# Kernel optimization log

Hardware: AMD Instinct MI355X
Metric: run time of the kernel (lower is better)

The kernel has to match this reference:

```python
import jax, jax.numpy as jnp
import numpy as np

B, C, D = 1024, 100000, 512
S_SCALE, MARGIN, EPS = 64.0, 0.5, 1e-7  # arcface defaults


def setup_inputs() -> dict:
    key = jax.random.key(0)
    kx, kl, kw = jax.random.split(key, 3)
    x = jax.random.normal(kx, (B, D), dtype=jnp.float32)
    labels = jax.random.randint(kl, (B,), 0, C, dtype=jnp.int64)
    # nn.Linear default init: U(-1/sqrt(fan_in), 1/sqrt(fan_in))
    bound = 1.0 / np.sqrt(D)
    W = jax.random.uniform(kw, (C, D), dtype=jnp.float32, minval=-bound, maxval=bound)
    return {"x": x, "labels": labels, "W": W}


def reference(x, labels, W):
    # L2-normalize features (W is NOT normalized in the original -- the
    # normalize loop there rebinds a local and is a no-op).
    xn = x / jnp.maximum(jnp.linalg.norm(x, axis=1, keepdims=True), 1e-12)
    wf = jnp.einsum('bd,cd->bc', xn, W)               # [B, C] cosine-like logits
    target = jnp.take_along_axis(wf, labels[:, None], axis=1)[:, 0]  # [B]
    # arcface: s * cos(acos(clamp(cos_theta)) + m)
    numerator = S_SCALE * jnp.cos(
        jnp.arccos(jnp.clip(target, -1.0 + EPS, 1.0 - EPS)) + MARGIN)
    # sum over excluded classes = full sum - label term
    excl_sum = jnp.sum(jnp.exp(S_SCALE * wf), axis=1) - jnp.exp(S_SCALE * target)
    L = numerator - jnp.log(jnp.exp(numerator) + excl_sum)
    return -jnp.mean(L)
```

## Files before the change

### kernel.cpp

```cpp
#include <hip/hip_runtime.h>
#include <hip/hip_bf16.h>
#include <math.h>

#define NB 1024
#define NC 100000
#define ND 512
#define SSCALE 64.0f
#define MMARGIN 0.5f

#define BM 256
#define BN 128
#define BK 32
#define NKS (ND / BK)
#define NRT (NB / BM)
#define NCT ((NC + BN - 1) / BN)
#define GRIDSZ (NRT * NCT)

#define ABASE 0
#define ABUF  16384
#define BBASE 32768
#define BBUF  8192

typedef __bf16 bf16x8 __attribute__((ext_vector_type(8)));
typedef float f32x4 __attribute__((ext_vector_type(4)));

__device__ __forceinline__ void gload_lds16(const void* g, void* l) {
    __builtin_amdgcn_global_load_lds(
        (const __attribute__((address_space(1))) unsigned int*)g,
        (__attribute__((address_space(3))) unsigned int*)l, 16, 0, 0);
}


__global__ void prep_kernel(const float* __restrict__ x, __bf16* __restrict__ xnb) {
    const int row = blockIdx.x;
    const int tid = threadIdx.x;
    const float2 v = *reinterpret_cast<const float2*>(x + (size_t)row * ND + tid * 2);
    float ss = v.x * v.x + v.y * v.y;
#pragma unroll
    for (int m = 1; m < 64; m <<= 1) ss += __shfl_xor(ss, m);
    __shared__ float wsum[4];
    if ((tid & 63) == 0) wsum[tid >> 6] = ss;
    __syncthreads();
    const float tot = wsum[0] + wsum[1] + wsum[2] + wsum[3];
    const float inv = 1.0f / fmaxf(sqrtf(tot), 1e-12f);
    __bf16* dst = xnb + (size_t)row * ND + tid * 2;
    dst[0] = (__bf16)(v.x * inv);
    dst[1] = (__bf16)(v.y * inv);
}

__global__ void target_kernel(const __bf16* __restrict__ xnb, const float* __restrict__ Wg,
                              const int* __restrict__ labels, float* __restrict__ tgt) {
    const int wid  = threadIdx.x >> 6;
    const int lane = threadIdx.x & 63;
    const int row  = blockIdx.x * 4 + wid;
    const int lab  = labels[row];
    const int k    = lane * 8;
    const bf16x8 xv = *reinterpret_cast<const bf16x8*>(xnb + (size_t)row * ND + k);
    const float* wr = Wg + (size_t)lab * ND + k;
    const float4 w0 = *reinterpret_cast<const float4*>(wr);
    const float4 w1 = *reinterpret_cast<const float4*>(wr + 4);
    float s = (float)xv[0] * w0.x + (float)xv[1] * w0.y + (float)xv[2] * w0.z + (float)xv[3] * w0.w
            + (float)xv[4] * w1.x + (float)xv[5] * w1.y + (float)xv[6] * w1.z + (float)xv[7] * w1.w;
#pragma unroll
    for (int m = 1; m < 64; m <<= 1) s += __shfl_xor(s, m);
    if (lane == 0) tgt[row] = s;
}

__global__ __launch_bounds__(512, 4) void gemm_exp_kernel(const __bf16* __restrict__ xnb,
                                                          const float* __restrict__ Wg,
                                                          float* __restrict__ sums) {
    __shared__ char lds[49152];
    const int tid  = threadIdx.x;
    const int wid  = tid >> 6;
    const int lane = tid & 63;
    const int l15  = lane & 15;
    const int lhi  = lane >> 4;
    const int wr   = wid >> 1;
    const int wc   = wid & 1;

    const int logical = (blockIdx.x & 7) * (GRIDSZ / 8) + (blockIdx.x >> 3);
    const int rt = logical & 3;
    const int ct = logical >> 2;
    const int r0 = rt * BM;
    const int c0 = ct * BN;

    const int bcls = tid >> 2;
    const int bqk  = tid & 3;
    const bool bok = (c0 + bcls) < NC;
    float4 bw0, bw1;
    auto loadB = [&](int t) {
        if (bok) {
            const float* src = Wg + (size_t)(c0 + bcls) * ND + t * BK + bqk * 8;
            bw0 = *reinterpret_cast<const float4*>(src);
            bw1 = *reinterpret_cast<const float4*>(src + 4);
        } else {
            bw0 = make_float4(0.f, 0.f, 0.f, 0.f);
            bw1 = bw0;
        }
    };
    auto writeB = [&](int buf) {
        struct alignas(16) bf8s { __bf16 h[8]; };
        bf8s h;
        h.h[0] = (__bf16)bw0.x; h.h[1] = (__bf16)bw0.y; h.h[2] = (__bf16)bw0.z; h.h[3] = (__bf16)bw0.w;
        h.h[4] = (__bf16)bw1.x; h.h[5] = (__bf16)bw1.y; h.h[6] = (__bf16)bw1.z; h.h[7] = (__bf16)bw1.w;
        const int ck = bqk ^ ((bcls >> 1) & 3);
        *reinterpret_cast<bf8s*>(lds + BBASE + buf * BBUF + bcls * 64 + (ck << 4)) = h;
    };

    auto stageA = [&](int t, int buf) {
#pragma unroll
        for (int s = 0; s < 2; ++s) {
            const int lin = s * 8192 + wid * 1024 + (lane << 4);
            const int row = lin >> 6;
            const int cnk = (lin >> 4) & 3;
            const int sc  = cnk ^ ((row >> 1) & 3);
            const char* src = (const char*)xnb + (size_t)(r0 + row) * 1024 + t * 64 + sc * 16;
            gload_lds16(src, lds + ABASE + buf * ABUF + s * 8192 + wid * 1024);
        }
    };

    f32x4 acc[4][4] = {};

    auto compute = [&](int buf) {
        bf16x8 a[4], b[4];
#pragma unroll
        for (int i = 0; i < 4; ++i) {
            const int r = wr * 64 + i * 16 + l15;
            const int ck = lhi ^ ((r >> 1) & 3);
            a[i] = *reinterpret_cast<const bf16x8*>(lds + ABASE + buf * ABUF + r * 64 + (ck << 4));
        }
#pragma unroll
        for (int j = 0; j < 4; ++j) {
            const int cls = wc * 64 + j * 16 + l15;
            const int ck  = lhi ^ ((cls >> 1) & 3);
            b[j] = *reinterpret_cast<const bf16x8*>(lds + BBASE + buf * BBUF + cls * 64 + (ck << 4));
        }
#pragma unroll
        for (int i = 0; i < 4; ++i)
#pragma unroll
            for (int j = 0; j < 4; ++j)
                acc[i][j] = __builtin_amdgcn_mfma_f32_16x16x32_bf16(a[i], b[j], acc[i][j], 0, 0, 0);
    };

    loadB(0);
    stageA(0, 0);
    writeB(0);
    __syncthreads();

#pragma unroll 1
    for (int t = 0; t < NKS; ++t) {
        const int buf = t & 1;
        if (t + 1 < NKS) {
            loadB(t + 1);
            stageA(t + 1, buf ^ 1);
        }
        compute(buf);
        if (t + 1 < NKS) writeB(buf ^ 1);
        __syncthreads();
    }

#pragma unroll
    for (int i = 0; i < 4; ++i) {
#pragma unroll
        for (int r = 0; r < 4; ++r) {
            float v = 0.f;
#pragma unroll
            for (int j = 0; j < 4; ++j) {
                const int c = c0 + wc * 64 + j * 16 + l15;
                v += (c < NC) ? __expf(SSCALE * acc[i][j][r]) : 0.f;
            }
            v += __shfl_xor(v, 1);
            v += __shfl_xor(v, 2);
            v += __shfl_xor(v, 4);
            v += __shfl_xor(v, 8);
            if (l15 == 0) {
                const int row = r0 + wr * 64 + i * 16 + lhi * 4 + r;
                atomicAdd(&sums[row], v);
            }
        }
    }
}

__global__ void finalize_kernel(const float* __restrict__ sums, const float* __restrict__ tgt,
                                float* __restrict__ out) {
    const int tid  = threadIdx.x;
    const int wid  = tid >> 6;
    const int lane = tid & 63;
    float t  = tgt[tid];
    const float se = sums[tid];
    t = fminf(fmaxf(t, -1.0f + 1e-7f), 1.0f - 1e-7f);
    const float numer = SSCALE * cosf(acosf(t) + MMARGIN);
    const float excl  = se - expf(SSCALE * t);
    float L = numer - logf(expf(numer) + excl);
#pragma unroll
    for (int m = 1; m < 64; m <<= 1) L += __shfl_xor(L, m);
    __shared__ float ws2[16];
    if (lane == 0) ws2[wid] = L;
    __syncthreads();
    if (tid == 0) {
        float tot = 0.f;
        for (int i = 0; i < 16; ++i) tot += ws2[i];
        out[0] = -(tot / (float)NB);
    }
}

extern "C" void kernel_launch(void* const* d_in, const int* in_sizes, int n_in,
                              void* d_out, int out_size, void* d_ws, size_t ws_size,
                              hipStream_t stream) {
    const float* x      = (const float*)d_in[0];
    const int*   labels = (const int*)d_in[1];
    const float* W      = (const float*)d_in[2];
    float* out = (float*)d_out;

    char* wsb = (char*)d_ws;
    __bf16* xnb  = (__bf16*)wsb;
    float*  sums = (float*)(wsb + (size_t)NB * ND * 2);
    float*  tgt  = sums + NB;

    hipMemsetAsync(sums, 0, NB * sizeof(float), stream);
    prep_kernel<<<NB, 256, 0, stream>>>(x, xnb);
    target_kernel<<<NB / 4, 256, 0, stream>>>(xnb, W, labels, tgt);
    gemm_exp_kernel<<<GRIDSZ, 512, 0, stream>>>(xnb, W, sums);
    finalize_kernel<<<1, 1024, 0, stream>>>(sums, tgt, out);
}
```

Measured before the change: 238.1 us.

## Pre-convert W to bf16 and stage B via direct-to-LDS loads with BK=64

```diff
diff --git a/kernel.cpp b/kernel.cpp
--- a/kernel.cpp
+++ b/kernel.cpp
@@ -10,16 +10,15 @@
 
 #define BM 256
 #define BN 128
-#define BK 32
+#define BK 64
 #define NKS (ND / BK)
 #define NRT (NB / BM)
 #define NCT ((NC + BN - 1) / BN)
 #define GRIDSZ (NRT * NCT)
-
-#define ABASE 0
-#define ABUF  16384
-#define BBASE 32768
-#define BBUF  8192
+#define NCPAD 100096
+
+#define ABUF  32768
+#define BBASE 65536
 
 typedef __bf16 bf16x8 __attribute__((ext_vector_type(8)));
 typedef float f32x4 __attribute__((ext_vector_type(4)));
@@ -66,10 +65,23 @@
     if (lane == 0) tgt[row] = s;
 }
 
-__global__ __launch_bounds__(512, 4) void gemm_exp_kernel(const __bf16* __restrict__ xnb,
-                                                          const float* __restrict__ Wg,
+__global__ void cvtw_kernel(const float* __restrict__ W, __bf16* __restrict__ Wbf) {
+    const size_t gid = (size_t)blockIdx.x * 256 + threadIdx.x;
+    bf16x8 h = {};
+    if (gid * 8 < (size_t)NC * ND) {
+        const float4 v0 = *reinterpret_cast<const float4*>(W + gid * 8);
+        const float4 v1 = *reinterpret_cast<const float4*>(W + gid * 8 + 4);
+        h[0] = (__bf16)v0.x; h[1] = (__bf16)v0.y; h[2] = (__bf16)v0.z; h[3] = (__bf16)v0.w;
+        h[4] = (__bf16)v1.x; h[5] = (__bf16)v1.y; h[6] = (__bf16)v1.z; h[7] = (__bf16)v1.w;
+    }
+    *reinterpret_cast<bf16x8*>(Wbf + gid * 8) = h;
+}
+
+template<int BMODE>
+__global__ __launch_bounds__(512, 2) void gemm_exp_kernel(const __bf16* __restrict__ xnb,
+                                                          const void* __restrict__ Bsrc,
                                                           float* __restrict__ sums) {
-    __shared__ char lds[49152];
+    __shared__ char lds[81920];
     const int tid  = threadIdx.x;
     const int wid  = tid >> 6;
     const int lane = tid & 63;
@@ -84,79 +96,105 @@
     const int r0 = rt * BM;
     const int c0 = ct * BN;
 
+    auto stageA = [&](int t, int buf) {
+#pragma unroll
+        for (int s = 0; s < 4; ++s) {
+            const int lin = s * 8192 + wid * 1024 + lane * 16;
+            const int row = lin >> 7;
+            const int cnk = (lin >> 4) & 7;
+            const int sc  = cnk ^ (row & 7);
+            const char* src = (const char*)xnb + (size_t)(r0 + row) * 1024 + t * 128 + sc * 16;
+            gload_lds16(src, lds + buf * ABUF + s * 8192 + wid * 1024);
+        }
+    };
+    auto stageB = [&](int t) {
+#pragma unroll
+        for (int g = 0; g < 2; ++g) {
+            const int lin = g * 8192 + wid * 1024 + lane * 16;
+            const int cls = lin >> 7;
+            const int cnk = (lin >> 4) & 7;
+            const int sc  = cnk ^ (cls & 7);
+            const char* src = (const char*)Bsrc + (size_t)(c0 + cls) * 1024 + t * 128 + sc * 16;
+            gload_lds16(src, lds + BBASE + g * 8192 + wid * 1024);
+        }
+    };
     const int bcls = tid >> 2;
-    const int bqk  = tid & 3;
-    const bool bok = (c0 + bcls) < NC;
-    float4 bw0, bw1;
+    const int bq   = tid & 3;
+    float4 bw[4];
     auto loadB = [&](int t) {
-        if (bok) {
-            const float* src = Wg + (size_t)(c0 + bcls) * ND + t * BK + bqk * 8;
-            bw0 = *reinterpret_cast<const float4*>(src);
-            bw1 = *reinterpret_cast<const float4*>(src + 4);
+        const float* src = (const float*)Bsrc + (size_t)(c0 + bcls) * ND + t * BK + bq * 16;
+        if (c0 + bcls < NC) {
+            bw[0] = *reinterpret_cast<const float4*>(src);
+            bw[1] = *reinterpret_cast<const float4*>(src + 4);
+            bw[2] = *reinterpret_cast<const float4*>(src + 8);
+            bw[3] = *reinterpret_cast<const float4*>(src + 12);
         } else {
-            bw0 = make_float4(0.f, 0.f, 0.f, 0.f);
-            bw1 = bw0;
-        }
-    };
-    auto writeB = [&](int buf) {
+            bw[0] = make_float4(0.f, 0.f, 0.f, 0.f);
+            bw[1] = bw[2] = bw[3] = bw[0];
+        }
+    };
+    auto writeB = [&]() {
         struct alignas(16) bf8s { __bf16 h[8]; };
-        bf8s h;
-        h.h[0] = (__bf16)bw0.x; h.h[1] = (__bf16)bw0.y; h.h[2] = (__bf16)bw0.z; h.h[3] = (__bf16)bw0.w;
-        h.h[4] = (__bf16)bw1.x; h.h[5] = (__bf16)bw1.y; h.h[6] = (__bf16)bw1.z; h.h[7] = (__bf16)bw1.w;
-        const int ck = bqk ^ ((bcls >> 1) & 3);
-        *reinterpret_cast<bf8s*>(lds + BBASE + buf * BBUF + bcls * 64 + (ck << 4)) = h;
-    };
-
-    auto stageA = [&](int t, int buf) {
-#pragma unroll
-        for (int s = 0; s < 2; ++s) {
-            const int lin = s * 8192 + wid * 1024 + (lane << 4);
-            const int row = lin >> 6;
-            const int cnk = (lin >> 4) & 3;
-            const int sc  = cnk ^ ((row >> 1) & 3);
-            const char* src = (const char*)xnb + (size_t)(r0 + row) * 1024 + t * 64 + sc * 16;
-            gload_lds16(src, lds + ABASE + buf * ABUF + s * 8192 + wid * 1024);
-        }
+        bf8s p0, p1;
+        p0.h[0] = (__bf16)bw[0].x; p0.h[1] = (__bf16)bw[0].y; p0.h[2] = (__bf16)bw[0].z; p0.h[3] = (__bf16)bw[0].w;
+        p0.h[4] = (__bf16)bw[1].x; p0.h[5] = (__bf16)bw[1].y; p0.h[6] = (__bf16)bw[1].z; p0.h[7] = (__bf16)bw[1].w;
+        p1.h[0] = (__bf16)bw[2].x; p1.h[1] = (__bf16)bw[2].y; p1.h[2] = (__bf16)bw[2].z; p1.h[3] = (__bf16)bw[2].w;
+        p1.h[4] = (__bf16)bw[3].x; p1.h[5] = (__bf16)bw[3].y; p1.h[6] = (__bf16)bw[3].z; p1.h[7] = (__bf16)bw[3].w;
+        char* base = lds + BBASE + bcls * 128;
+        *reinterpret_cast<bf8s*>(base + (((bq * 2)     ^ (bcls & 7)) << 4)) = p0;
+        *reinterpret_cast<bf8s*>(base + (((bq * 2 + 1) ^ (bcls & 7)) << 4)) = p1;
     };
 
     f32x4 acc[4][4] = {};
 
     auto compute = [&](int buf) {
-        bf16x8 a[4], b[4];
-#pragma unroll
-        for (int i = 0; i < 4; ++i) {
-            const int r = wr * 64 + i * 16 + l15;
-            const int ck = lhi ^ ((r >> 1) & 3);
-            a[i] = *reinterpret_cast<const bf16x8*>(lds + ABASE + buf * ABUF + r * 64 + (ck << 4));
-        }
-#pragma unroll
-        for (int j = 0; j < 4; ++j) {
-            const int cls = wc * 64 + j * 16 + l15;
-            const int ck  = lhi ^ ((cls >> 1) & 3);
-            b[j] = *reinterpret_cast<const bf16x8*>(lds + BBASE + buf * BBUF + cls * 64 + (ck << 4));
-        }
-#pragma unroll
-        for (int i = 0; i < 4; ++i)
-#pragma unroll
-            for (int j = 0; j < 4; ++j)
-                acc[i][j] = __builtin_amdgcn_mfma_f32_16x16x32_bf16(a[i], b[j], acc[i][j], 0, 0, 0);
-    };
-
-    loadB(0);
+#pragma unroll
+        for (int kk = 0; kk < 2; ++kk) {
+            bf16x8 a[4], b[4];
+            const int ck = (kk << 2) | lhi;
+#pragma unroll
+            for (int i = 0; i < 4; ++i) {
+                const int r = wr * 64 + i * 16 + l15;
+                a[i] = *reinterpret_cast<const bf16x8*>(
+                    lds + buf * ABUF + r * 128 + ((ck ^ (r & 7)) << 4));
+            }
+#pragma unroll
+            for (int j = 0; j < 4; ++j) {
+                const int cls = wc * 64 + j * 16 + l15;
+                b[j] = *reinterpret_cast<const bf16x8*>(
+                    lds + BBASE + cls * 128 + ((ck ^ (cls & 7)) << 4));
+            }
+#pragma unroll
+            for (int i = 0; i < 4; ++i)
+#pragma unroll
+                for (int j = 0; j < 4; ++j)
+                    acc[i][j] = __builtin_amdgcn_mfma_f32_16x16x32_bf16(a[i], b[j], acc[i][j], 0, 0, 0);
+        }
+    };
+
     stageA(0, 0);
-    writeB(0);
+    if constexpr (BMODE == 0) {
+        stageB(0);
+    } else {
+        loadB(0);
+        writeB();
+    }
     __syncthreads();
 
 #pragma unroll 1
     for (int t = 0; t < NKS; ++t) {
         const int buf = t & 1;
         if (t + 1 < NKS) {
-            loadB(t + 1);
             stageA(t + 1, buf ^ 1);
+            if constexpr (BMODE == 1) loadB(t + 1);
         }
         compute(buf);
-        if (t + 1 < NKS) writeB(buf ^ 1);
-        __syncthreads();
+        if (t + 1 < NKS) {
+            __syncthreads();
+            if constexpr (BMODE == 0) stageB(t + 1);
+            else                      writeB();
+            __syncthreads();
+        }
     }
 
 #pragma unroll
@@ -214,12 +252,19 @@
 
     char* wsb = (char*)d_ws;
     __bf16* xnb  = (__bf16*)wsb;
-    float*  sums = (float*)(wsb + (size_t)NB * ND * 2);
-    float*  tgt  = sums + NB;
+    float*  sums = (float*)(wsb + 1048576);
+    float*  tgt  = (float*)(wsb + 1052672);
+    __bf16* Wbf  = (__bf16*)(wsb + 1056768);
+    const size_t WS_NEED = 1056768ull + (size_t)NCPAD * ND * 2;
 
     hipMemsetAsync(sums, 0, NB * sizeof(float), stream);
     prep_kernel<<<NB, 256, 0, stream>>>(x, xnb);
     target_kernel<<<NB / 4, 256, 0, stream>>>(xnb, W, labels, tgt);
-    gemm_exp_kernel<<<GRIDSZ, 512, 0, stream>>>(xnb, W, sums);
+    if (ws_size >= WS_NEED) {
+        cvtw_kernel<<<((size_t)NCPAD * ND) / (256 * 8), 256, 0, stream>>>(W, Wbf);
+        gemm_exp_kernel<0><<<GRIDSZ, 512, 0, stream>>>(xnb, Wbf, sums);
+    } else {
+        gemm_exp_kernel<1><<<GRIDSZ, 512, 0, stream>>>(xnb, W, sums);
+    }
     finalize_kernel<<<1, 1024, 0, stream>>>(sums, tgt, out);
 }
```

Result: slower. 243.1 us (+2.1%).
